# Optimization experiments

Measured on AMD Instinct MI355X. Metric: run time of the kernel, lower is better.

## Reference

```python
import jax, jax.numpy as jnp
import numpy as np

B, LQ, LK, D = 32, 1024, 1024, 256

def setup_inputs() -> dict:
    key = jax.random.key(0)
    ks = jax.random.split(key, 7)
    return {
        "raw_query": jax.random.normal(ks[0], (B, LQ, D), dtype=jnp.float32),
        "raw_key": jax.random.normal(ks[1], (B, LK, D), dtype=jnp.float32),
        "raw_value": jax.random.normal(ks[2], (B, LK, D), dtype=jnp.float32),
        "value_mask": jax.random.randint(ks[3], (B, LQ), 0, 2, dtype=jnp.int32),
        "WQ": jax.random.normal(ks[4], (D, D), dtype=jnp.float32) * 0.05,
        "WK": jax.random.normal(ks[5], (D, D), dtype=jnp.float32) * 0.05,
        "WV": jax.random.normal(ks[6], (D, D), dtype=jnp.float32) * 0.05,
    }

def reference(raw_query, raw_key, raw_value, value_mask, WQ, WK, WV):
    # Projections: [B, L, D] @ [D, D]
    Q = raw_query @ WQ
    K = raw_key @ WK
    V = raw_value @ WV
    # Scores: [B, LQ, LK] (use_scale=False -> no 1/sqrt(d_k))
    att = jnp.einsum("bqd,bkd->bqk", Q, K)
    # Mask expanded on axis=2 -> zeroes entire query rows of scores (faithful to tf.where+zeros_like)
    att = jnp.where(value_mask[:, :, None] > 0, att, jnp.zeros((), dtype=att.dtype))
    att = jax.nn.softmax(att, axis=-1)
    # Output: [B, LQ, D]
    return jnp.einsum("bqk,bkd->bqd", att, V)
```

## Files before the change

### kernel.cpp

```cpp
#include <hip/hip_runtime.h>
#include <hip/hip_bf16.h>
#include <math.h>

#define B_ 32
#define L_ 1024
#define D_ 256

typedef _Float16 half8 __attribute__((ext_vector_type(8)));
typedef __fp16   fp16x2 __attribute__((ext_vector_type(2)));
typedef short    s16x8 __attribute__((ext_vector_type(8)));
typedef float    f32x4 __attribute__((ext_vector_type(4)));

typedef __attribute__((address_space(3))) unsigned int lds_u32;
typedef __attribute__((address_space(1))) unsigned int gbl_u32;

__device__ __forceinline__ void gl_lds16(const void* g, void* l) {
    __builtin_amdgcn_global_load_lds((gbl_u32*)g, (lds_u32*)l, 16, 0, 0);
}

__device__ __forceinline__ unsigned short f2bf(float x) {
    unsigned u = __float_as_uint(x);
    u += 0x7FFFu + ((u >> 16) & 1u);
    return (unsigned short)(u >> 16);
}

__device__ __forceinline__ unsigned short f2h(float x) {
    _Float16 h = (_Float16)x;
    unsigned short u;
    __builtin_memcpy(&u, &h, 2);
    return u;
}

__device__ __forceinline__ unsigned pkrtz(float a, float b) {
    fp16x2 v = __builtin_amdgcn_cvt_pkrtz(a, b);
    unsigned u;
    __builtin_memcpy(&u, &v, 4);
    return u;
}

__global__ __launch_bounds__(256) void wprep_kernel(
    const float* __restrict__ W0, const float* __restrict__ W1,
    const float* __restrict__ W2, unsigned short* __restrict__ Wt)
{
    const int z = blockIdx.z;
    const float* __restrict__ W = (z == 0) ? W0 : (z == 1) ? W1 : W2;
    __shared__ unsigned short T[64][72];
    const int k0 = blockIdx.x << 6, n0 = blockIdx.y << 6;
    const int t = threadIdx.x;
    const int r = t >> 2, c0 = (t & 3) << 4;
    #pragma unroll
    for (int j = 0; j < 16; j += 4) {
        float4 w4 = *(const float4*)(W + (size_t)(k0 + r) * 256 + n0 + c0 + j);
        T[c0 + j + 0][r] = f2h(w4.x);
        T[c0 + j + 1][r] = f2h(w4.y);
        T[c0 + j + 2][r] = f2h(w4.z);
        T[c0 + j + 3][r] = f2h(w4.w);
    }
    __syncthreads();
    const int n = t >> 2, kc = (t & 3) << 4;
    unsigned short* dst = Wt + ((size_t)z << 16) + (size_t)(n0 + n) * 256 + k0 + kc;
    *(uint4*)(dst + 0) = *(const uint4*)&T[n][kc + 0];
    *(uint4*)(dst + 8) = *(const uint4*)&T[n][kc + 8];
}

__global__ __launch_bounds__(256) void proj_mfma_kernel(
    const float* __restrict__ A0, const float* __restrict__ A1,
    const float* __restrict__ A2, const unsigned short* __restrict__ Wt,
    unsigned short* __restrict__ Qh, unsigned short* __restrict__ Kh,
    unsigned short* __restrict__ Vt)
{
    __shared__ unsigned short SMEM[32768];
    unsigned short* Asm = SMEM;
    unsigned short* Bsm = SMEM + 16384;

    const int z = blockIdx.z;
    const float* __restrict__ A = (z == 0) ? A0 : (z == 1) ? A1 : A2;
    const int bm = blockIdx.x << 7, bn = blockIdx.y << 7;
    const int t = threadIdx.x, lane = t & 63, w = t >> 6;
    const int wm = (w >> 1) << 6, wn = (w & 1) << 6;

    const float* __restrict__ Ag = A + (size_t)bm * 256;
    const unsigned short* __restrict__ Bg = Wt + ((size_t)z << 16) + (size_t)bn * 256;

    f32x4 acc[4][4];
    const f32x4 z4 = {0.f, 0.f, 0.f, 0.f};
    #pragma unroll
    for (int mi = 0; mi < 4; ++mi)
        #pragma unroll
        for (int ni = 0; ni < 4; ++ni) acc[mi][ni] = z4;

    float4 a_reg[8];

    auto loadA = [&](int it) {
        #pragma unroll
        for (int i = 0; i < 8; ++i) {
            int r  = (t >> 4) + (i << 4);
            int c4 = t & 15;
            a_reg[i] = *(const float4*)(Ag + (size_t)r * 256 + (it << 6) + (c4 << 2));
        }
    };
    auto writeA = [&](int buf) {
        #pragma unroll
        for (int i = 0; i < 8; ++i) {
            int r  = (t >> 4) + (i << 4);
            int c4 = t & 15;
            unsigned h01 = pkrtz(a_reg[i].x, a_reg[i].y);
            unsigned h23 = pkrtz(a_reg[i].z, a_reg[i].w);
            int cs = (c4 >> 1) ^ (r & 7);
            uint2 d2; d2.x = h01; d2.y = h23;
            *(uint2*)&Asm[(buf << 13) + (r << 6) + (cs << 3) + ((c4 & 1) << 2)] = d2;
        }
    };
    auto stageB = [&](int buf, int it) {
        #pragma unroll
        for (int rr = 0; rr < 4; ++rr) {
            int o = (rr << 8) + t;
            int r = o >> 3, c = o & 7;
            int cs = c ^ (r & 7);
            gl_lds16(Bg + (size_t)r * 256 + (it << 6) + (cs << 3),
                     &Bsm[(buf << 13) + (o << 3)]);
        }
    };
    auto compute = [&](int buf) {
        #pragma unroll
        for (int kc = 0; kc < 2; ++kc) {
            half8 af[4], bfr[4];
            #pragma unroll
            for (int mi = 0; mi < 4; ++mi) {
                int m = wm + (mi << 4) + (lane & 15);
                int cs = ((kc << 2) + (lane >> 4)) ^ (m & 7);
                af[mi] = *(const half8*)&Asm[(buf << 13) + (m << 6) + (cs << 3)];
            }
            #pragma unroll
            for (int ni = 0; ni < 4; ++ni) {
                int n = wn + (ni << 4) + (lane & 15);
                int cs = ((kc << 2) + (lane >> 4)) ^ (n & 7);
                bfr[ni] = *(const half8*)&Bsm[(buf << 13) + (n << 6) + (cs << 3)];
            }
            #pragma unroll
            for (int mi = 0; mi < 4; ++mi)
                #pragma unroll
                for (int ni = 0; ni < 4; ++ni)
                    acc[mi][ni] = __builtin_amdgcn_mfma_f32_16x16x32_f16(
                        af[mi], bfr[ni], acc[mi][ni], 0, 0, 0);
        }
    };

    loadA(0);
    writeA(0);
    stageB(0, 0);
    loadA(1);
    __syncthreads();

    for (int it = 0; it < 4; ++it) {
        const int buf = it & 1;
        if (it < 3) {
            stageB(buf ^ 1, it + 1);
            writeA(buf ^ 1);
            if (it < 2) loadA(it + 2);
        }
        compute(buf);
        __syncthreads();
    }

    if (z < 2) {
        unsigned short* __restrict__ C = (z == 0) ? Qh : Kh;
        #pragma unroll
        for (int mi = 0; mi < 4; ++mi) {
            int q = bm + wm + (mi << 4) + ((lane >> 4) << 2);
            #pragma unroll
            for (int ni = 0; ni < 4; ++ni) {
                int col = bn + wn + (ni << 4) + (lane & 15);
                #pragma unroll
                for (int r = 0; r < 4; ++r)
                    C[(size_t)(q + r) * 256 + col] = f2h(acc[mi][ni][r]);
            }
        }
    } else {
        __syncthreads();
        unsigned short (*Tt)[144] = (unsigned short(*)[144])SMEM;
        #pragma unroll
        for (int mi = 0; mi < 4; ++mi) {
            #pragma unroll
            for (int ni = 0; ni < 4; ++ni) {
                int n  = wn + (ni << 4) + (lane & 15);
                int m0 = wm + (mi << 4) + ((lane >> 4) << 2);
                ushort4 v;
                v.x = f2bf(acc[mi][ni][0]);
                v.y = f2bf(acc[mi][ni][1]);
                v.z = f2bf(acc[mi][ni][2]);
                v.w = f2bf(acc[mi][ni][3]);
                *(ushort4*)&Tt[n][m0] = v;
            }
        }
        __syncthreads();
        const int bb = bm >> 10, kin = bm & 1023;
        const int dr = t >> 1, cb = (t & 1) << 6;
        unsigned short* dst = Vt + ((size_t)bb * 256 + bn + dr) * 1024 + kin + cb;
        #pragma unroll
        for (int j = 0; j < 8; ++j)
            *(uint4*)(dst + (j << 3)) = *(const uint4*)&Tt[dr][cb + (j << 3)];
    }
}

__global__ __launch_bounds__(1024, 4) void fused_attn_kernel(
    const unsigned short* __restrict__ Qh, const unsigned short* __restrict__ Kh,
    const unsigned short* __restrict__ Vt, const int* __restrict__ mask,
    float* __restrict__ Out)
{
    __shared__ unsigned short Ks[2][16384];
    __shared__ unsigned short Vs[2][16384];
    __shared__ unsigned short Ps[128 * 64];
    float* lredp = (float*)Ps;

    const int f  = blockIdx.x;
    const int b  = (f & 7) + ((f >> 6) << 3);
    const int q0 = ((f >> 3) & 7) << 7;
    const size_t bL = (size_t)b * L_;
    const int t = threadIdx.x, lane = t & 63, w = t >> 6;
    const int wm_s = (w >> 1) << 4, wn_s = (w & 1) << 5;
    const int wm_v = (w >> 2) << 5, wn_v = (w & 3) << 6;

    const unsigned short* __restrict__ Kb = Kh + (bL << 8);
    const unsigned short* __restrict__ Vb = Vt + (bL << 8);

    auto stageK = [&](int buf, int kt) {
        #pragma unroll
        for (int i = 0; i < 2; ++i) {
            int o = (i << 10) + t;
            int r = o >> 5, c = o & 31;
            int cs = (c & 24) | ((c & 7) ^ (r & 7));
            gl_lds16(Kb + (size_t)((kt << 6) + r) * 256 + (cs << 3), &Ks[buf][o << 3]);
        }
    };
    auto stageV = [&](int buf, int kt) {
        #pragma unroll
        for (int i = 0; i < 2; ++i) {
            int o = (i << 10) + t;
            int d = o >> 3, c = o & 7;
            int cs = c ^ (d & 7);
            gl_lds16(Vb + ((size_t)d << 10) + (kt << 6) + (cs << 3), &Vs[buf][o << 3]);
        }
    };

    stageK(0, 0);
    stageV(0, 0);

    half8 qf[8];
    {
        int m = wm_s + (lane & 15);
        const unsigned short* qp = Qh + ((bL + q0 + m) << 8) + ((lane >> 4) << 3);
        #pragma unroll
        for (int kc = 0; kc < 8; ++kc)
            qf[kc] = *(const half8*)(qp + (kc << 5));
    }
    int mv[4];
    {
        int qrow = wm_s + ((lane >> 4) << 2);
        #pragma unroll
        for (int r = 0; r < 4; ++r) mv[r] = mask[bL + q0 + qrow + r];
    }

    f32x4 o_acc[2][4];
    const f32x4 z4 = {0.f, 0.f, 0.f, 0.f};
    #pragma unroll
    for (int mi = 0; mi < 2; ++mi)
        #pragma unroll
        for (int ni = 0; ni < 4; ++ni) o_acc[mi][ni] = z4;
    float lacc[4] = {};

    __syncthreads();

    for (int kt = 0; kt < 16; ++kt) {
        const int cur = kt & 1;
        if (kt < 15) stageV(cur ^ 1, kt + 1);

        f32x4 accs[2];
        accs[0] = z4; accs[1] = z4;
        #pragma unroll
        for (int kc = 0; kc < 8; ++kc) {
            int kb = (kc >> 1) << 6, cc = ((kc & 1) << 2) + (lane >> 4);
            int n0 = wn_s + (lane & 15);
            int n1 = n0 + 16;
            half8 bf0 = *(const half8*)&Ks[cur][(n0 << 8) + kb + ((cc ^ (n0 & 7)) << 3)];
            half8 bf1 = *(const half8*)&Ks[cur][(n1 << 8) + kb + ((cc ^ (n1 & 7)) << 3)];
            accs[0] = __builtin_amdgcn_mfma_f32_16x16x32_f16(qf[kc], bf0, accs[0], 0, 0, 0);
            accs[1] = __builtin_amdgcn_mfma_f32_16x16x32_f16(qf[kc], bf1, accs[1], 0, 0, 0);
        }

        {
            int qrow = wm_s + ((lane >> 4) << 2);
            #pragma unroll
            for (int ni = 0; ni < 2; ++ni) {
                int kl = wn_s + (ni << 4) + (lane & 15);
                #pragma unroll
                for (int r = 0; r < 4; ++r) {
                    int q = qrow + r;
                    float p = mv[r] ? __expf(accs[ni][r]) : 1.0f;
                    Ps[(q << 6) + ((((kl >> 3) ^ (q & 7)) << 3)) + (kl & 7)] = f2bf(p);
                    lacc[r] += p;
                }
            }
        }
        __syncthreads();

        if (kt < 15) stageK(cur ^ 1, kt + 1);

        #pragma unroll
        for (int kc2 = 0; kc2 < 2; ++kc2) {
            s16x8 pa[2], vb[4];
            int cc = (kc2 << 2) + (lane >> 4);
            #pragma unroll
            for (int mi = 0; mi < 2; ++mi) {
                int m = wm_v + (mi << 4) + (lane & 15);
                pa[mi] = *(const s16x8*)&Ps[(m << 6) + ((cc ^ (m & 7)) << 3)];
            }
            #pragma unroll
            for (int ni = 0; ni < 4; ++ni) {
                int n = wn_v + (ni << 4) + (lane & 15);
                vb[ni] = *(const s16x8*)&Vs[cur][(n << 6) + ((cc ^ (n & 7)) << 3)];
            }
            #pragma unroll
            for (int mi = 0; mi < 2; ++mi)
                #pragma unroll
                for (int ni = 0; ni < 4; ++ni)
                    o_acc[mi][ni] = __builtin_amdgcn_mfma_f32_16x16x32_bf16(
                        pa[mi], vb[ni], o_acc[mi][ni], 0, 0, 0);
        }
        __syncthreads();
    }

    #pragma unroll
    for (int r = 0; r < 4; ++r) {
        float v = lacc[r];
        v += __shfl_xor(v, 1);
        v += __shfl_xor(v, 2);
        v += __shfl_xor(v, 4);
        v += __shfl_xor(v, 8);
        if ((lane & 15) == 0)
            lredp[((wm_s + ((lane >> 4) << 2) + r) << 1) + (w & 1)] = v;
    }
    __syncthreads();

    #pragma unroll
    for (int mi = 0; mi < 2; ++mi) {
        #pragma unroll
        for (int rr = 0; rr < 4; ++rr) {
            int q = wm_v + (mi << 4) + ((lane >> 4) << 2) + rr;
            float inv = 1.0f / (lredp[q << 1] + lredp[(q << 1) + 1]);
            #pragma unroll
            for (int ni = 0; ni < 4; ++ni) {
                int d = wn_v + (ni << 4) + (lane & 15);
                Out[((bL + q0 + q) << 8) + d] = o_acc[mi][ni][rr] * inv;
            }
        }
    }
}

extern "C" void kernel_launch(void* const* d_in, const int* in_sizes, int n_in,
                              void* d_out, int out_size, void* d_ws, size_t ws_size,
                              hipStream_t stream) {
    const float* rq = (const float*)d_in[0];
    const float* rk = (const float*)d_in[1];
    const float* rv = (const float*)d_in[2];
    const int*   vm = (const int*)d_in[3];
    const float* WQ = (const float*)d_in[4];
    const float* WK = (const float*)d_in[5];
    const float* WV = (const float*)d_in[6];
    float* out = (float*)d_out;

    char* ws = (char*)d_ws;
    unsigned short* Qh = (unsigned short*)(ws);
    unsigned short* Kh = (unsigned short*)(ws + ((size_t)16 << 20));
    unsigned short* Vt = (unsigned short*)(ws + ((size_t)32 << 20));
    unsigned short* Wt = (unsigned short*)(ws + ((size_t)48 << 20));

    dim3 wg(4, 4, 3);
    wprep_kernel<<<wg, 256, 0, stream>>>(WQ, WK, WV, Wt);

    dim3 pg(256, 2, 3);
    proj_mfma_kernel<<<pg, 256, 0, stream>>>(rq, rk, rv, Wt, Qh, Kh, Vt);

    fused_attn_kernel<<<256, 1024, 0, stream>>>(Qh, Kh, Vt, vm, out);
}
```

Measured before the change: 91.51 us.

## Halve projection K-tile to 32 and raise occupancy to four blocks per CU

```diff
diff --git a/kernel.cpp b/kernel.cpp
--- a/kernel.cpp
+++ b/kernel.cpp
@@ -63,15 +63,15 @@
     *(uint4*)(dst + 8) = *(const uint4*)&T[n][kc + 8];
 }
 
-__global__ __launch_bounds__(256) void proj_mfma_kernel(
+__global__ __launch_bounds__(256, 4) void proj_mfma_kernel(
     const float* __restrict__ A0, const float* __restrict__ A1,
     const float* __restrict__ A2, const unsigned short* __restrict__ Wt,
     unsigned short* __restrict__ Qh, unsigned short* __restrict__ Kh,
     unsigned short* __restrict__ Vt)
 {
-    __shared__ unsigned short SMEM[32768];
+    __shared__ unsigned short SMEM[18432];
     unsigned short* Asm = SMEM;
-    unsigned short* Bsm = SMEM + 16384;
+    unsigned short* Bsm = SMEM + 8192;
 
     const int z = blockIdx.z;
     const float* __restrict__ A = (z == 0) ? A0 : (z == 1) ? A1 : A2;
@@ -89,61 +89,62 @@
         #pragma unroll
         for (int ni = 0; ni < 4; ++ni) acc[mi][ni] = z4;
 
-    float4 a_reg[8];
+    const int ar = t >> 1, ach = t & 1;
+    float4 a_reg[4];
 
     auto loadA = [&](int it) {
         #pragma unroll
-        for (int i = 0; i < 8; ++i) {
-            int r  = (t >> 4) + (i << 4);
-            int c4 = t & 15;
-            a_reg[i] = *(const float4*)(Ag + (size_t)r * 256 + (it << 6) + (c4 << 2));
-        }
+        for (int i = 0; i < 4; ++i)
+            a_reg[i] = *(const float4*)(Ag + (size_t)ar * 256 + (it << 5) + (ach << 4) + (i << 2));
     };
     auto writeA = [&](int buf) {
-        #pragma unroll
-        for (int i = 0; i < 8; ++i) {
-            int r  = (t >> 4) + (i << 4);
-            int c4 = t & 15;
-            unsigned h01 = pkrtz(a_reg[i].x, a_reg[i].y);
-            unsigned h23 = pkrtz(a_reg[i].z, a_reg[i].w);
-            int cs = (c4 >> 1) ^ (r & 7);
-            uint2 d2; d2.x = h01; d2.y = h23;
-            *(uint2*)&Asm[(buf << 13) + (r << 6) + (cs << 3) + ((c4 & 1) << 2)] = d2;
+        unsigned h[8];
+        #pragma unroll
+        for (int i = 0; i < 4; ++i) {
+            h[2 * i]     = pkrtz(a_reg[i].x, a_reg[i].y);
+            h[2 * i + 1] = pkrtz(a_reg[i].z, a_reg[i].w);
+        }
+        int swz = (ar + (ar >> 2)) & 3;
+        #pragma unroll
+        for (int jj = 0; jj < 2; ++jj) {
+            int cs = ((ach << 1) + jj) ^ swz;
+            uint2 d0; d0.x = h[4 * jj + 0]; d0.y = h[4 * jj + 1];
+            uint2 d1; d1.x = h[4 * jj + 2]; d1.y = h[4 * jj + 3];
+            *(uint2*)&Asm[(buf << 12) + (ar << 5) + (cs << 3) + 0] = d0;
+            *(uint2*)&Asm[(buf << 12) + (ar << 5) + (cs << 3) + 4] = d1;
         }
     };
     auto stageB = [&](int buf, int it) {
         #pragma unroll
-        for (int rr = 0; rr < 4; ++rr) {
-            int o = (rr << 8) + t;
-            int r = o >> 3, c = o & 7;
-            int cs = c ^ (r & 7);
-            gl_lds16(Bg + (size_t)r * 256 + (it << 6) + (cs << 3),
-                     &Bsm[(buf << 13) + (o << 3)]);
+        for (int i = 0; i < 2; ++i) {
+            int o = (i << 8) + t;
+            int r = o >> 2, c = o & 3;
+            int cs = c ^ ((r + (r >> 2)) & 3);
+            gl_lds16(Bg + (size_t)r * 256 + (it << 5) + (cs << 3),
+                     &Bsm[(buf << 12) + (o << 3)]);
         }
     };
     auto compute = [&](int buf) {
-        #pragma unroll
-        for (int kc = 0; kc < 2; ++kc) {
-            half8 af[4], bfr[4];
-            #pragma unroll
-            for (int mi = 0; mi < 4; ++mi) {
-                int m = wm + (mi << 4) + (lane & 15);
-                int cs = ((kc << 2) + (lane >> 4)) ^ (m & 7);
-                af[mi] = *(const half8*)&Asm[(buf << 13) + (m << 6) + (cs << 3)];
-            }
-            #pragma unroll
-            for (int ni = 0; ni < 4; ++ni) {
-                int n = wn + (ni << 4) + (lane & 15);
-                int cs = ((kc << 2) + (lane >> 4)) ^ (n & 7);
-                bfr[ni] = *(const half8*)&Bsm[(buf << 13) + (n << 6) + (cs << 3)];
-            }
-            #pragma unroll
-            for (int mi = 0; mi < 4; ++mi)
-                #pragma unroll
-                for (int ni = 0; ni < 4; ++ni)
-                    acc[mi][ni] = __builtin_amdgcn_mfma_f32_16x16x32_f16(
-                        af[mi], bfr[ni], acc[mi][ni], 0, 0, 0);
-        }
+        half8 af[4], bfr[4];
+        const int cc = lane >> 4;
+        #pragma unroll
+        for (int mi = 0; mi < 4; ++mi) {
+            int m = wm + (mi << 4) + (lane & 15);
+            int cs = cc ^ ((m + (m >> 2)) & 3);
+            af[mi] = *(const half8*)&Asm[(buf << 12) + (m << 5) + (cs << 3)];
+        }
+        #pragma unroll
+        for (int ni = 0; ni < 4; ++ni) {
+            int n = wn + (ni << 4) + (lane & 15);
+            int cs = cc ^ ((n + (n >> 2)) & 3);
+            bfr[ni] = *(const half8*)&Bsm[(buf << 12) + (n << 5) + (cs << 3)];
+        }
+        #pragma unroll
+        for (int mi = 0; mi < 4; ++mi)
+            #pragma unroll
+            for (int ni = 0; ni < 4; ++ni)
+                acc[mi][ni] = __builtin_amdgcn_mfma_f32_16x16x32_f16(
+                    af[mi], bfr[ni], acc[mi][ni], 0, 0, 0);
     };
 
     loadA(0);
@@ -152,12 +153,12 @@
     loadA(1);
     __syncthreads();
 
-    for (int it = 0; it < 4; ++it) {
+    for (int it = 0; it < 8; ++it) {
         const int buf = it & 1;
-        if (it < 3) {
+        if (it < 7) {
             stageB(buf ^ 1, it + 1);
             writeA(buf ^ 1);
-            if (it < 2) loadA(it + 2);
+            if (it < 6) loadA(it + 2);
         }
         compute(buf);
         __syncthreads();
```

New measurement: 89.69 us. 1.02x faster.

## Swizzle projection grid for XCD L2 locality and deepen A-load prefetch

Applied to the files above, without the earlier changes.

```diff
diff --git a/kernel.cpp b/kernel.cpp
--- a/kernel.cpp
+++ b/kernel.cpp
@@ -73,9 +73,17 @@
     unsigned short* Asm = SMEM;
     unsigned short* Bsm = SMEM + 16384;
 
-    const int z = blockIdx.z;
+    const int fblk = blockIdx.x;
+    const int xcd = fblk & 7;
+    const int g   = fblk >> 3;
+    const int y   = g & 1;
+    const int p   = g >> 1;
+    const int z   = p >> 5;
+    const int xl  = p & 31;
+    const int xt  = (xcd << 5) + xl;
+    const int bm = xt << 7, bn = y << 7;
+
     const float* __restrict__ A = (z == 0) ? A0 : (z == 1) ? A1 : A2;
-    const int bm = blockIdx.x << 7, bn = blockIdx.y << 7;
     const int t = threadIdx.x, lane = t & 63, w = t >> 6;
     const int wm = (w >> 1) << 6, wn = (w & 1) << 6;
 
@@ -89,28 +97,31 @@
         #pragma unroll
         for (int ni = 0; ni < 4; ++ni) acc[mi][ni] = z4;
 
-    float4 a_reg[8];
-
-    auto loadA = [&](int it) {
-        #pragma unroll
-        for (int i = 0; i < 8; ++i) {
-            int r  = (t >> 4) + (i << 4);
-            int c4 = t & 15;
-            a_reg[i] = *(const float4*)(Ag + (size_t)r * 256 + (it << 6) + (c4 << 2));
-        }
-    };
-    auto writeA = [&](int buf) {
-        #pragma unroll
-        for (int i = 0; i < 8; ++i) {
-            int r  = (t >> 4) + (i << 4);
-            int c4 = t & 15;
-            unsigned h01 = pkrtz(a_reg[i].x, a_reg[i].y);
-            unsigned h23 = pkrtz(a_reg[i].z, a_reg[i].w);
-            int cs = (c4 >> 1) ^ (r & 7);
-            uint2 d2; d2.x = h01; d2.y = h23;
-            *(uint2*)&Asm[(buf << 13) + (r << 6) + (cs << 3) + ((c4 & 1) << 2)] = d2;
-        }
-    };
+    float4 aA[8], aB[8];
+
+#define LOADA(itv, AR)                                                          \
+    {                                                                           \
+        _Pragma("unroll")                                                       \
+        for (int i = 0; i < 8; ++i) {                                           \
+            int r  = (t >> 4) + (i << 4);                                       \
+            int c4 = t & 15;                                                    \
+            AR[i] = *(const float4*)(Ag + (size_t)r * 256 + ((itv) << 6) + (c4 << 2)); \
+        }                                                                       \
+    }
+#define WRITEA(buf, AR)                                                         \
+    {                                                                           \
+        _Pragma("unroll")                                                       \
+        for (int i = 0; i < 8; ++i) {                                           \
+            int r  = (t >> 4) + (i << 4);                                       \
+            int c4 = t & 15;                                                    \
+            unsigned h01 = pkrtz(AR[i].x, AR[i].y);                             \
+            unsigned h23 = pkrtz(AR[i].z, AR[i].w);                             \
+            int cs = (c4 >> 1) ^ (r & 7);                                       \
+            uint2 d2; d2.x = h01; d2.y = h23;                                   \
+            *(uint2*)&Asm[((buf) << 13) + (r << 6) + (cs << 3) + ((c4 & 1) << 2)] = d2; \
+        }                                                                       \
+    }
+
     auto stageB = [&](int buf, int it) {
         #pragma unroll
         for (int rr = 0; rr < 4; ++rr) {
@@ -146,22 +157,30 @@
         }
     };
 
-    loadA(0);
-    writeA(0);
+    LOADA(0, aA);
+    WRITEA(0, aA);
     stageB(0, 0);
-    loadA(1);
-    __syncthreads();
-
-    for (int it = 0; it < 4; ++it) {
-        const int buf = it & 1;
-        if (it < 3) {
-            stageB(buf ^ 1, it + 1);
-            writeA(buf ^ 1);
-            if (it < 2) loadA(it + 2);
-        }
-        compute(buf);
-        __syncthreads();
-    }
+    LOADA(1, aB);
+    __syncthreads();
+
+    LOADA(2, aA);
+    WRITEA(1, aB);
+    stageB(1, 1);
+    compute(0);
+    __syncthreads();
+    LOADA(3, aB);
+    WRITEA(0, aA);
+    stageB(0, 2);
+    compute(1);
+    __syncthreads();
+    WRITEA(1, aB);
+    stageB(1, 3);
+    compute(0);
+    __syncthreads();
+    compute(1);
+
+#undef LOADA
+#undef WRITEA
 
     if (z < 2) {
         unsigned short* __restrict__ C = (z == 0) ? Qh : Kh;
@@ -378,8 +397,7 @@
     dim3 wg(4, 4, 3);
     wprep_kernel<<<wg, 256, 0, stream>>>(WQ, WK, WV, Wt);
 
-    dim3 pg(256, 2, 3);
-    proj_mfma_kernel<<<pg, 256, 0, stream>>>(rq, rk, rv, Wt, Qh, Kh, Vt);
+    proj_mfma_kernel<<<1536, 256, 0, stream>>>(rq, rk, rv, Wt, Qh, Kh, Vt);
 
     fused_attn_kernel<<<256, 1024, 0, stream>>>(Qh, Kh, Vt, vm, out);
 }
```

After: 89.94 us. No clear change (-1.7%).
